# Kernel optimization log

Hardware: AMD Instinct MI355X
Metric: run time of the kernel (lower is better)

The kernel has to match this reference:

```python
import jax, jax.numpy as jnp
import numpy as np
from jax import lax

DS = 4  # downsample_factor

def setup_inputs() -> dict:
    key = jax.random.key(0)
    ks = jax.random.split(key, 7)
    B, C, H, W = 4, 256, 256, 256
    Cq = C // 16  # reduction=16
    return {
        "x":  jax.random.normal(ks[0], (B, C, H, W), dtype=jnp.float32),
        "Wq": jax.random.normal(ks[1], (Cq, C), dtype=jnp.float32) * 0.05,
        "bq": jax.random.normal(ks[2], (Cq,), dtype=jnp.float32) * 0.05,
        "Wk": jax.random.normal(ks[3], (Cq, C), dtype=jnp.float32) * 0.05,
        "bk": jax.random.normal(ks[4], (Cq,), dtype=jnp.float32) * 0.05,
        "Wv": jax.random.normal(ks[5], (C, C), dtype=jnp.float32) * 0.05,
        "bv": jax.random.normal(ks[6], (C,), dtype=jnp.float32) * 0.05,
    }

def reference(x, Wq, bq, Wk, bk, Wv, bv):
    B, C, H, W = x.shape
    # MaxPool2d(kernel=DS, stride=DS)
    xd = lax.reduce_window(x, -jnp.inf, lax.max,
                           (1, 1, DS, DS), (1, 1, DS, DS), 'VALID')
    h, w = xd.shape[2], xd.shape[3]
    N = h * w
    # 1x1 convs == channel-wise linear maps
    q = jnp.einsum('oc,bchw->bohw', Wq, xd) + bq[None, :, None, None]
    k = jnp.einsum('oc,bchw->bohw', Wk, xd) + bk[None, :, None, None]
    v = jnp.einsum('oc,bchw->bohw', Wv, xd) + bv[None, :, None, None]
    query = q.reshape(B, -1, N).transpose(0, 2, 1)   # [B, N, Cq]
    key_  = k.reshape(B, -1, N)                      # [B, Cq, N]
    value = v.reshape(B, C, N).transpose(0, 2, 1)    # [B, N, C]
    att = jnp.einsum('bnc,bcm->bnm', query, key_)    # [B, N, N]
    # global-mean threshold masking (zeros, not -inf, per original)
    att = jnp.where(att < att.mean(), 0.0, att)
    att = jax.nn.softmax(att, axis=-1)
    out = jnp.einsum('bnm,bmc->bnc', att, value)     # [B, N, C]
    out = out.transpose(0, 2, 1).reshape(B, C, h, w)
    # bilinear upsample, align_corners=False (half-pixel centers)
    out = jax.image.resize(out, (B, C, H, W), method='bilinear')
    return out + x
```

## Files before the change

kernel.cpp:

```cpp
#include <hip/hip_runtime.h>
#include <hip/hip_bf16.h>
#include <cmath>
#include <cstdint>
#include <cstddef>

typedef unsigned short u16;
typedef __attribute__((ext_vector_type(8))) __bf16 bf16x8;
typedef __attribute__((ext_vector_type(4))) float f32x4;
typedef __attribute__((ext_vector_type(8))) unsigned short us8;
typedef __attribute__((ext_vector_type(4))) unsigned short us4;

static const size_t OFF_XD32  = 0;
static const size_t OFF_QT    = 16777216;
static const size_t OFF_KT    = 17825792;
static const size_t OFF_VT    = 18874368;
static const size_t OFF_WF    = 27262976;
static const size_t OFF_SPART = 27394048;
static const size_t OFF_MEAN  = 27426816;

__device__ __forceinline__ void gl2lds16(const void* gsrc, void* ldst) {
  __builtin_amdgcn_global_load_lds(
      (const __attribute__((address_space(1))) unsigned int*)gsrc,
      (__attribute__((address_space(3))) unsigned int*)ldst, 16, 0, 0);
}

__device__ __forceinline__ float hmax4(float4 v) {
  return fmaxf(fmaxf(v.x, v.y), fmaxf(v.z, v.w));
}

__global__ __launch_bounds__(256) void k_prepw(const float* __restrict__ Wv,
                                               u16* __restrict__ Wf) {
  const int rt = blockIdx.x;
  const int tid = threadIdx.x;
#pragma unroll
  for (int i = 0; i < 2; ++i) {
    int s = tid + i * 256;
    int ks = s >> 6, lane = s & 63;
    const float* src = Wv + (size_t)(rt * 16 + (lane & 15)) * 256u + ks * 32 + (lane >> 4) * 8;
    float4 a = *reinterpret_cast<const float4*>(src);
    float4 b = *reinterpret_cast<const float4*>(src + 4);
    us8 o;
    o[0] = __builtin_bit_cast(u16, __float2bfloat16(a.x));
    o[1] = __builtin_bit_cast(u16, __float2bfloat16(a.y));
    o[2] = __builtin_bit_cast(u16, __float2bfloat16(a.z));
    o[3] = __builtin_bit_cast(u16, __float2bfloat16(a.w));
    o[4] = __builtin_bit_cast(u16, __float2bfloat16(b.x));
    o[5] = __builtin_bit_cast(u16, __float2bfloat16(b.y));
    o[6] = __builtin_bit_cast(u16, __float2bfloat16(b.z));
    o[7] = __builtin_bit_cast(u16, __float2bfloat16(b.w));
    *reinterpret_cast<us8*>(Wf + ((size_t)((rt * 8 + ks) * 64 + lane)) * 8u) = o;
  }
}

__global__ __launch_bounds__(256) void k_pool(const float* __restrict__ x,
                                              float* __restrict__ xd32) {
  unsigned idx = blockIdx.x * 256u + threadIdx.x;
  unsigned xo = idx & 63u;
  unsigned yo = (idx >> 6) & 63u;
  unsigned bc = idx >> 12;
  const float* base = x + (size_t)bc * 65536u + yo * 1024u + xo * 4u;
  float m = -1e30f;
#pragma unroll
  for (int dy = 0; dy < 4; ++dy) {
    float4 v = *reinterpret_cast<const float4*>(base + dy * 256);
    m = fmaxf(m, hmax4(v));
  }
  xd32[(size_t)bc * 4096u + yo * 64u + xo] = m;
}

__global__ __launch_bounds__(512) void k_qk(const float* __restrict__ xd32,
                                            const float* __restrict__ Wq, const float* __restrict__ bq,
                                            const float* __restrict__ Wk, const float* __restrict__ bk,
                                            float* __restrict__ qT, float* __restrict__ kT,
                                            float* __restrict__ Spart) {
  __shared__ float xs[256][64];
  const int blk = blockIdx.x;
  const int b = blk >> 6, n0 = (blk & 63) * 64;
  const int tid = threadIdx.x;
  {
    const float* src = xd32 + (size_t)b * 1048576u + n0;
#pragma unroll
    for (int i = 0; i < 8; ++i) {
      int slot = tid + i * 512;
      int c = slot >> 4, q4 = slot & 15;
      *reinterpret_cast<float4*>(&xs[c][q4 * 4]) =
          *reinterpret_cast<const float4*>(src + (size_t)c * 4096u + q4 * 4);
    }
  }
  __syncthreads();
  const int o = tid >> 4, t4 = tid & 15;
  const float* wrow = (o < 16) ? (Wq + (size_t)o * 256u) : (Wk + (size_t)(o - 16) * 256u);
  float a0 = 0.f, a1 = 0.f, a2 = 0.f, a3 = 0.f;
  for (int c = 0; c < 256; ++c) {
    float w = wrow[c];
    float4 xv = *reinterpret_cast<const float4*>(&xs[c][t4 * 4]);
    a0 = fmaf(w, xv.x, a0);
    a1 = fmaf(w, xv.y, a1);
    a2 = fmaf(w, xv.z, a2);
    a3 = fmaf(w, xv.w, a3);
  }
  float* dst = (o < 16) ? qT : kT;
  int oo = (o < 16) ? o : (o - 16);
  float bb = (o < 16) ? bq[oo] : bk[oo];
  size_t base = ((size_t)b * 4096u + n0 + t4 * 4) * 16u + oo;
  dst[base]      = a0 + bb;
  dst[base + 16] = a1 + bb;
  dst[base + 32] = a2 + bb;
  dst[base + 48] = a3 + bb;
  float s = a0 + a1 + a2 + a3;
  s += __shfl_xor(s, 1); s += __shfl_xor(s, 2);
  s += __shfl_xor(s, 4); s += __shfl_xor(s, 8);
  if (t4 == 0) Spart[(size_t)blk * 32u + o] = s;
}

__global__ __launch_bounds__(256) void k_vgemm(const float* __restrict__ xd32,
                                               const u16* __restrict__ Wf,
                                               const float* __restrict__ bv,
                                               u16* __restrict__ vT) {
  __shared__ u16 Bf[4][8][64][8];
  const int blk = blockIdx.x;
  const int b = blk >> 6, n0 = (blk & 63) * 64;
  const int tid = threadIdx.x;
  const int w = tid >> 6, lane = tid & 63;

#pragma unroll
  for (int p = 0; p < 16; ++p) {
    int idx = p * 256 + tid;
    int k = idx >> 4, q4 = idx & 15;
    float4 v = *reinterpret_cast<const float4*>(
        xd32 + ((size_t)b * 256 + k) * 4096u + n0 + q4 * 4);
    int ks = k >> 5, kl = (k >> 3) & 3, j = k & 7;
    int ct = q4 >> 2, nb = (q4 & 3) * 4;
    Bf[ct][ks][kl * 16 + nb + 0][j] = __builtin_bit_cast(u16, __float2bfloat16(v.x));
    Bf[ct][ks][kl * 16 + nb + 1][j] = __builtin_bit_cast(u16, __float2bfloat16(v.y));
    Bf[ct][ks][kl * 16 + nb + 2][j] = __builtin_bit_cast(u16, __float2bfloat16(v.z));
    Bf[ct][ks][kl * 16 + nb + 3][j] = __builtin_bit_cast(u16, __float2bfloat16(v.w));
  }
  __syncthreads();

  f32x4 acc[4][4];
#pragma unroll
  for (int r = 0; r < 4; ++r)
#pragma unroll
    for (int ct = 0; ct < 4; ++ct) acc[r][ct] = (f32x4){0.f, 0.f, 0.f, 0.f};
  for (int ks = 0; ks < 8; ++ks) {
    bf16x8 Bv[4];
#pragma unroll
    for (int ct = 0; ct < 4; ++ct)
      Bv[ct] = __builtin_bit_cast(bf16x8, *reinterpret_cast<const us8*>(&Bf[ct][ks][lane][0]));
#pragma unroll
    for (int r = 0; r < 4; ++r) {
      int rt = w * 4 + r;
      bf16x8 Av = __builtin_bit_cast(bf16x8,
          *reinterpret_cast<const us8*>(Wf + ((size_t)((rt * 8 + ks) * 64 + lane)) * 8u));
#pragma unroll
      for (int ct = 0; ct < 4; ++ct)
        acc[r][ct] = __builtin_amdgcn_mfma_f32_16x16x32_bf16(Av, Bv[ct], acc[r][ct], 0, 0, 0);
    }
  }

#pragma unroll
  for (int r = 0; r < 4; ++r) {
    int row0 = (w * 4 + r) * 16 + (lane >> 4) * 4;
#pragma unroll
    for (int rr = 0; rr < 4; ++rr) {
      int c = row0 + rr;
      float bb = bv[c];
      u16* dst = vT + ((size_t)b * 256 + c) * 4096u + n0 + (lane & 15);
#pragma unroll
      for (int ct = 0; ct < 4; ++ct)
        dst[ct * 16] = __builtin_bit_cast(u16, __float2bfloat16(acc[r][ct][rr] + bb));
    }
  }
}

__global__ __launch_bounds__(64) void k_mean(const float* __restrict__ Spart,
                                             const float* __restrict__ bq, const float* __restrict__ bk,
                                             float* __restrict__ meanp) {
  int t = threadIdx.x;
  int b = t >> 4, o = t & 15;
  float sq = 4096.0f * bq[o], sk = 4096.0f * bk[o];
  for (int blk = 0; blk < 64; ++blk) {
    const float* p = Spart + ((size_t)(b * 64 + blk)) * 32u;
    sq += p[o];
    sk += p[16 + o];
  }
  float pr = sq * sk;
#pragma unroll
  for (int off = 32; off > 0; off >>= 1) pr += __shfl_down(pr, off);
  if (t == 0) *meanp = pr * (1.0f / 67108864.0f);
}

__global__ __launch_bounds__(512) void k_flash(const float* __restrict__ qT,
                                               const float* __restrict__ kT,
                                               const u16* __restrict__ vT,
                                               const float* __restrict__ meanp,
                                               float* __restrict__ ods) {
  __shared__ u16 vbuf[2][16384];
  __shared__ u16 kfh[2][4][64][8];
  __shared__ u16 kfl[2][4][64][8];
  __shared__ u16 pfr[8][2][64][8];

  const int orig = blockIdx.x;
  const int b    = (orig >> 1) & 3;
  const int row0 = (((orig & 1) << 5) | (orig >> 3)) * 64;
  const int tid  = threadIdx.x;
  const int w    = tid >> 6;
  const int lane = tid & 63;
  const int wq   = w & 3;
  const int wc   = w >> 2;
  const int g    = lane >> 4;
  const int c16  = lane & 15;

  const float mean = *meanp;

  float qv[16];
  {
    const float* qrow = qT + ((size_t)b*4096 + row0 + 16*wq + c16) * 16;
#pragma unroll
    for (int i = 0; i < 4; ++i) {
      float4 t4 = reinterpret_cast<const float4*>(qrow)[i];
      qv[4*i] = t4.x; qv[4*i+1] = t4.y; qv[4*i+2] = t4.z; qv[4*i+3] = t4.w;
    }
  }
  u16 qhi[16], qlo[16];
#pragma unroll
  for (int i = 0; i < 16; ++i) {
    __hip_bfloat16 h = __float2bfloat16(qv[i]);
    float fh = __bfloat162float(h);
    __hip_bfloat16 lo = __float2bfloat16(qv[i] - fh);
    qhi[i] = __builtin_bit_cast(u16, h);
    qlo[i] = __builtin_bit_cast(u16, lo);
  }
  us8 a1u, a2u;
  {
    const bool koff8  = (g & 1);
    const bool lo_src = (g >= 2);
#pragma unroll
    for (int i = 0; i < 8; ++i) {
      u16 hs = koff8 ? qhi[i+8] : qhi[i];
      u16 ls = koff8 ? qlo[i+8] : qlo[i];
      a1u[i] = lo_src ? ls : hs;
      a2u[i] = lo_src ? (u16)0 : hs;
    }
  }
  const bf16x8 A1 = __builtin_bit_cast(bf16x8, a1u);
  const bf16x8 A2 = __builtin_bit_cast(bf16x8, a2u);

  f32x4 O[8];
#pragma unroll
  for (int i = 0; i < 8; ++i) O[i] = (f32x4){0.f, 0.f, 0.f, 0.f};
  float Lr[4] = {0.f, 0.f, 0.f, 0.f};
  float M = 0.0f;

  const int kv_s = tid >> 2, t4v = tid & 3;
  const int ks = kv_s >> 4, kld0 = (kv_s & 15) + 16*(t4v >> 1), ki0 = 4*(t4v & 1);

  {
    const u16* vsrc = vT + (size_t)b*256*4096;
#pragma unroll
    for (int i = 0; i < 4; ++i) {
      int u = i*512 + tid;
      int row = u >> 3, slot = u & 7;
      int sb = (slot*16) ^ ((row & 7) << 4);
      gl2lds16((const char*)(vsrc + (size_t)row*4096) + sb, (char*)&vbuf[0][0] + u*16);
    }
    if (tid < 256) {
      float4 kvec = *reinterpret_cast<const float4*>(kT + ((size_t)b*4096 + kv_s)*16 + 4*t4v);
      float kf[4] = {kvec.x, kvec.y, kvec.z, kvec.w};
      us4 h4, l4;
#pragma unroll
      for (int di = 0; di < 4; ++di) {
        __hip_bfloat16 h = __float2bfloat16(kf[di]);
        float fh = __bfloat162float(h);
        __hip_bfloat16 lo = __float2bfloat16(kf[di] - fh);
        h4[di] = __builtin_bit_cast(u16, h);
        l4[di] = __builtin_bit_cast(u16, lo);
      }
      *reinterpret_cast<us4*>(&kfh[0][ks][kld0][ki0])    = h4;
      *reinterpret_cast<us4*>(&kfh[0][ks][kld0+32][ki0]) = h4;
      *reinterpret_cast<us4*>(&kfl[0][ks][kld0][ki0])    = l4;
      *reinterpret_cast<us4*>(&kfl[0][ks][kld0+32][ki0]) = l4;
    }
  }
  __syncthreads();

  for (int t = 0; t < 64; ++t) {
    const int cur = t & 1, nxt = cur ^ 1;
    const int kv0n = ((t + 1) & 63) * 64;

    float4 kvec;
    if (tid < 256)
      kvec = *reinterpret_cast<const float4*>(kT + ((size_t)b*4096 + kv0n + kv_s)*16 + 4*t4v);
    {
      const u16* vsrc = vT + (size_t)b*256*4096 + kv0n;
#pragma unroll
      for (int i = 0; i < 4; ++i) {
        int u = i*512 + tid;
        int row = u >> 3, slot = u & 7;
        int sb = (slot*16) ^ ((row & 7) << 4);
        gl2lds16((const char*)(vsrc + (size_t)row*4096) + sb, (char*)&vbuf[nxt][0] + u*16);
      }
    }

    f32x4 S[4];
#pragma unroll
    for (int s = 0; s < 4; ++s) {
      bf16x8 bh = __builtin_bit_cast(bf16x8, *reinterpret_cast<const us8*>(&kfh[cur][s][lane][0]));
      bf16x8 bl = __builtin_bit_cast(bf16x8, *reinterpret_cast<const us8*>(&kfl[cur][s][lane][0]));
      f32x4 acc = (f32x4){0.f, 0.f, 0.f, 0.f};
      acc = __builtin_amdgcn_mfma_f32_16x16x32_bf16(A1, bh, acc, 0, 0, 0);
      acc = __builtin_amdgcn_mfma_f32_16x16x32_bf16(A2, bl, acc, 0, 0, 0);
      S[s] = acc;
    }

    float pmax = -1e30f;
#pragma unroll
    for (int s = 0; s < 4; ++s)
#pragma unroll
      for (int r = 0; r < 4; ++r) {
        float v = S[s][r];
        v = (v < mean) ? 0.f : v;
        S[s][r] = v;
        pmax = fmaxf(pmax, v);
      }
    if (!__all(pmax <= M + 8.0f)) {
      float mw = pmax;
#pragma unroll
      for (int off = 1; off < 64; off <<= 1) mw = fmaxf(mw, __shfl_xor(mw, off));
      float Mn = fmaxf(M, mw);
      float sc = __expf(M - Mn);
#pragma unroll
      for (int i = 0; i < 8; ++i) {
        O[i][0] *= sc; O[i][1] *= sc; O[i][2] *= sc; O[i][3] *= sc;
      }
#pragma unroll
      for (int r = 0; r < 4; ++r) Lr[r] *= sc;
      M = Mn;
    }
    u16 pb[4][4];
#pragma unroll
    for (int s = 0; s < 4; ++s)
#pragma unroll
      for (int r = 0; r < 4; ++r) {
        float p = __expf(S[s][r] - M);
        Lr[r] += p;
        pb[s][r] = __builtin_bit_cast(u16, __float2bfloat16(p));
      }

    {
      const int ib = lane & 7;
      const int t1 = (lane >> 3) & 1;
#pragma unroll
      for (int s = 0; s < 4; ++s) {
        const int c2 = s >> 1;
        const int ldb = 16 * ((2*s + t1) & 3) + 4*g;
#pragma unroll
        for (int r = 0; r < 4; ++r) pfr[w][c2][ldb + r][ib] = pb[s][r];
      }
    }
    asm volatile("s_waitcnt lgkmcnt(0)" ::: "memory");
    __builtin_amdgcn_sched_barrier(0);

#pragma unroll
    for (int c2 = 0; c2 < 2; ++c2) {
      bf16x8 pa = __builtin_bit_cast(bf16x8, *reinterpret_cast<const us8*>(&pfr[w][c2][lane][0]));
#pragma unroll
      for (int ct = 0; ct < 8; ++ct) {
        int row = (wc*8 + ct)*16 + c16;
        int off = (c2*64 + g*16) ^ ((lane & 7) << 4);
        bf16x8 vb = __builtin_bit_cast(bf16x8,
            *reinterpret_cast<const us8*>((const char*)&vbuf[cur][0] + row*128 + off));
        O[ct] = __builtin_amdgcn_mfma_f32_16x16x32_bf16(pa, vb, O[ct], 0, 0, 0);
      }
    }

    if (tid < 256) {
      float kf[4] = {kvec.x, kvec.y, kvec.z, kvec.w};
      us4 h4, l4;
#pragma unroll
      for (int di = 0; di < 4; ++di) {
        __hip_bfloat16 h = __float2bfloat16(kf[di]);
        float fh = __bfloat162float(h);
        __hip_bfloat16 lo = __float2bfloat16(kf[di] - fh);
        h4[di] = __builtin_bit_cast(u16, h);
        l4[di] = __builtin_bit_cast(u16, lo);
      }
      *reinterpret_cast<us4*>(&kfh[nxt][ks][kld0][ki0])    = h4;
      *reinterpret_cast<us4*>(&kfh[nxt][ks][kld0+32][ki0]) = h4;
      *reinterpret_cast<us4*>(&kfl[nxt][ks][kld0][ki0])    = l4;
      *reinterpret_cast<us4*>(&kfl[nxt][ks][kld0+32][ki0]) = l4;
    }

    __syncthreads();
  }

#pragma unroll
  for (int r = 0; r < 4; ++r) {
    float v = Lr[r];
#pragma unroll
    for (int off = 1; off < 16; off <<= 1) v += __shfl_xor(v, off);
    Lr[r] = v;
  }
  float inv[4];
#pragma unroll
  for (int r = 0; r < 4; ++r) inv[r] = 1.0f / Lr[r];
#pragma unroll
  for (int ct = 0; ct < 8; ++ct) {
    int c = (wc*8 + ct)*16 + c16;
    float* dst = ods + ((size_t)b*256 + c) * 4096u + row0 + 16*wq + 4*g;
    float4 o4 = make_float4(O[ct][0]*inv[0], O[ct][1]*inv[1], O[ct][2]*inv[2], O[ct][3]*inv[3]);
    *reinterpret_cast<float4*>(dst) = o4;
  }
}

__global__ __launch_bounds__(256) void k_up(const float* __restrict__ ods, const float* __restrict__ x,
                                            float* __restrict__ out) {
  unsigned idx4 = blockIdx.x * 256u + threadIdx.x;
  int a  = (int)(idx4 & 63u);
  int i  = (int)((idx4 >> 6) & 255u);
  size_t bc = idx4 >> 14;

  float py = (i + 0.5f) * 0.25f - 0.5f;
  float y0f = floorf(py);
  float wy = py - y0f;
  int y0 = (int)y0f, y1 = y0 + 1;
  y0 = max(y0, 0); y1 = min(y1, 63);

  int xm1 = max(a - 1, 0), xp1 = min(a + 1, 63);

  const float* r0 = ods + bc * 4096u + y0 * 64;
  const float* r1 = ods + bc * 4096u + y1 * 64;
  float wy1 = 1.f - wy;
  float vm1 = wy1 * r0[xm1] + wy * r1[xm1];
  float v0  = wy1 * r0[a]   + wy * r1[a];
  float vp1 = wy1 * r0[xp1] + wy * r1[xp1];

  float4 xv = *reinterpret_cast<const float4*>(x + (size_t)idx4 * 4u);
  float4 o4;
  o4.x = fmaf(0.375f, vm1, 0.625f * v0) + xv.x;
  o4.y = fmaf(0.125f, vm1, 0.875f * v0) + xv.y;
  o4.z = fmaf(0.875f, v0, 0.125f * vp1) + xv.z;
  o4.w = fmaf(0.625f, v0, 0.375f * vp1) + xv.w;
  *reinterpret_cast<float4*>(out + (size_t)idx4 * 4u) = o4;
}

extern "C" void kernel_launch(void* const* d_in, const int* in_sizes, int n_in,
                              void* d_out, int out_size, void* d_ws, size_t ws_size,
                              hipStream_t stream) {
  const float* x  = (const float*)d_in[0];
  const float* Wq = (const float*)d_in[1];
  const float* bq = (const float*)d_in[2];
  const float* Wk = (const float*)d_in[3];
  const float* bk = (const float*)d_in[4];
  const float* Wv = (const float*)d_in[5];
  const float* bv = (const float*)d_in[6];
  float* out = (float*)d_out;

  char* ws = (char*)d_ws;
  float* xd32  = (float*)(ws + OFF_XD32);
  float* qT    = (float*)(ws + OFF_QT);
  float* kT    = (float*)(ws + OFF_KT);
  u16*   vT    = (u16*)(ws + OFF_VT);
  u16*   Wf    = (u16*)(ws + OFF_WF);
  float* Spart = (float*)(ws + OFF_SPART);
  float* mnp   = (float*)(ws + OFF_MEAN);
  float* ods   = xd32;

  k_prepw<<<dim3(16), dim3(256), 0, stream>>>(Wv, Wf);
  k_pool<<<dim3(16384), dim3(256), 0, stream>>>(x, xd32);
  k_qk<<<dim3(256), dim3(512), 0, stream>>>(xd32, Wq, bq, Wk, bk, qT, kT, Spart);
  k_vgemm<<<dim3(256), dim3(256), 0, stream>>>(xd32, Wf, bv, vT);
  k_mean<<<dim3(1), dim3(64), 0, stream>>>(Spart, bq, bk, mnp);
  k_flash<<<dim3(256), dim3(512), 0, stream>>>(qT, kT, vT, mnp, ods);
  k_up<<<dim3(65536), dim3(256), 0, stream>>>(ods, x, out);
}
```

Before: 286.6 us.

## Merge QK and V projection kernels and fold mean reduction into flash kernel

Combines the Q/K projection and V GEMM into one launch of 512 blocks, with the first 256 blocks doing V (now 512 threads, two row tiles per wave) and the rest doing Q/K. The separate single-block mean kernel is removed, and each flash block recomputes the global mean from the partial sums in shared memory. This is meant to cut two kernel launches and the tiny serial mean kernel, and to let the two projections run concurrently. In exchange, every flash block redundantly reads the partial sums, and the merged kernel reserves 64KB of shared memory for the V blocks, which needed less before, which may lower occupancy.

```diff
diff --git a/kernel.cpp b/kernel.cpp
--- a/kernel.cpp
+++ b/kernel.cpp
@@ -16,7 +16,6 @@
 static const size_t OFF_VT    = 18874368;
 static const size_t OFF_WF    = 27262976;
 static const size_t OFF_SPART = 27394048;
-static const size_t OFF_MEAN  = 27426816;
 
 __device__ __forceinline__ void gl2lds16(const void* gsrc, void* ldst) {
   __builtin_amdgcn_global_load_lds(
@@ -68,138 +67,123 @@
   xd32[(size_t)bc * 4096u + yo * 64u + xo] = m;
 }
 
-__global__ __launch_bounds__(512) void k_qk(const float* __restrict__ xd32,
-                                            const float* __restrict__ Wq, const float* __restrict__ bq,
-                                            const float* __restrict__ Wk, const float* __restrict__ bk,
-                                            float* __restrict__ qT, float* __restrict__ kT,
-                                            float* __restrict__ Spart) {
-  __shared__ float xs[256][64];
-  const int blk = blockIdx.x;
-  const int b = blk >> 6, n0 = (blk & 63) * 64;
+__global__ __launch_bounds__(512) void k_qkv(const float* __restrict__ xd32,
+                                             const u16* __restrict__ Wf, const float* __restrict__ bv,
+                                             const float* __restrict__ Wq, const float* __restrict__ bq,
+                                             const float* __restrict__ Wk, const float* __restrict__ bk,
+                                             float* __restrict__ qT, float* __restrict__ kT,
+                                             u16* __restrict__ vT, float* __restrict__ Spart) {
+  __shared__ char smem[65536];
   const int tid = threadIdx.x;
-  {
-    const float* src = xd32 + (size_t)b * 1048576u + n0;
-#pragma unroll
-    for (int i = 0; i < 8; ++i) {
-      int slot = tid + i * 512;
-      int c = slot >> 4, q4 = slot & 15;
-      *reinterpret_cast<float4*>(&xs[c][q4 * 4]) =
-          *reinterpret_cast<const float4*>(src + (size_t)c * 4096u + q4 * 4);
-    }
-  }
-  __syncthreads();
-  const int o = tid >> 4, t4 = tid & 15;
-  const float* wrow = (o < 16) ? (Wq + (size_t)o * 256u) : (Wk + (size_t)(o - 16) * 256u);
-  float a0 = 0.f, a1 = 0.f, a2 = 0.f, a3 = 0.f;
-  for (int c = 0; c < 256; ++c) {
-    float w = wrow[c];
-    float4 xv = *reinterpret_cast<const float4*>(&xs[c][t4 * 4]);
-    a0 = fmaf(w, xv.x, a0);
-    a1 = fmaf(w, xv.y, a1);
-    a2 = fmaf(w, xv.z, a2);
-    a3 = fmaf(w, xv.w, a3);
-  }
-  float* dst = (o < 16) ? qT : kT;
-  int oo = (o < 16) ? o : (o - 16);
-  float bb = (o < 16) ? bq[oo] : bk[oo];
-  size_t base = ((size_t)b * 4096u + n0 + t4 * 4) * 16u + oo;
-  dst[base]      = a0 + bb;
-  dst[base + 16] = a1 + bb;
-  dst[base + 32] = a2 + bb;
-  dst[base + 48] = a3 + bb;
-  float s = a0 + a1 + a2 + a3;
-  s += __shfl_xor(s, 1); s += __shfl_xor(s, 2);
-  s += __shfl_xor(s, 4); s += __shfl_xor(s, 8);
-  if (t4 == 0) Spart[(size_t)blk * 32u + o] = s;
-}
-
-__global__ __launch_bounds__(256) void k_vgemm(const float* __restrict__ xd32,
-                                               const u16* __restrict__ Wf,
-                                               const float* __restrict__ bv,
-                                               u16* __restrict__ vT) {
-  __shared__ u16 Bf[4][8][64][8];
-  const int blk = blockIdx.x;
-  const int b = blk >> 6, n0 = (blk & 63) * 64;
-  const int tid = threadIdx.x;
-  const int w = tid >> 6, lane = tid & 63;
-
-#pragma unroll
-  for (int p = 0; p < 16; ++p) {
-    int idx = p * 256 + tid;
-    int k = idx >> 4, q4 = idx & 15;
-    float4 v = *reinterpret_cast<const float4*>(
-        xd32 + ((size_t)b * 256 + k) * 4096u + n0 + q4 * 4);
-    int ks = k >> 5, kl = (k >> 3) & 3, j = k & 7;
-    int ct = q4 >> 2, nb = (q4 & 3) * 4;
-    Bf[ct][ks][kl * 16 + nb + 0][j] = __builtin_bit_cast(u16, __float2bfloat16(v.x));
-    Bf[ct][ks][kl * 16 + nb + 1][j] = __builtin_bit_cast(u16, __float2bfloat16(v.y));
-    Bf[ct][ks][kl * 16 + nb + 2][j] = __builtin_bit_cast(u16, __float2bfloat16(v.z));
-    Bf[ct][ks][kl * 16 + nb + 3][j] = __builtin_bit_cast(u16, __float2bfloat16(v.w));
-  }
-  __syncthreads();
-
-  f32x4 acc[4][4];
-#pragma unroll
-  for (int r = 0; r < 4; ++r)
-#pragma unroll
-    for (int ct = 0; ct < 4; ++ct) acc[r][ct] = (f32x4){0.f, 0.f, 0.f, 0.f};
-  for (int ks = 0; ks < 8; ++ks) {
-    bf16x8 Bv[4];
-#pragma unroll
-    for (int ct = 0; ct < 4; ++ct)
-      Bv[ct] = __builtin_bit_cast(bf16x8, *reinterpret_cast<const us8*>(&Bf[ct][ks][lane][0]));
-#pragma unroll
-    for (int r = 0; r < 4; ++r) {
-      int rt = w * 4 + r;
-      bf16x8 Av = __builtin_bit_cast(bf16x8,
-          *reinterpret_cast<const us8*>(Wf + ((size_t)((rt * 8 + ks) * 64 + lane)) * 8u));
+
+  if (blockIdx.x < 256) {
+    u16 (*Bf)[8][64][8] = reinterpret_cast<u16(*)[8][64][8]>(smem);
+    const int blk = blockIdx.x;
+    const int b = blk >> 6, n0 = (blk & 63) * 64;
+    const int w = tid >> 6, lane = tid & 63;
+
+#pragma unroll
+    for (int p = 0; p < 8; ++p) {
+      int idx = p * 512 + tid;
+      int k = idx >> 4, q4 = idx & 15;
+      float4 v = *reinterpret_cast<const float4*>(
+          xd32 + ((size_t)b * 256 + k) * 4096u + n0 + q4 * 4);
+      int ks = k >> 5, kl = (k >> 3) & 3, j = k & 7;
+      int ct = q4 >> 2, nb = (q4 & 3) * 4;
+      Bf[ct][ks][kl * 16 + nb + 0][j] = __builtin_bit_cast(u16, __float2bfloat16(v.x));
+      Bf[ct][ks][kl * 16 + nb + 1][j] = __builtin_bit_cast(u16, __float2bfloat16(v.y));
+      Bf[ct][ks][kl * 16 + nb + 2][j] = __builtin_bit_cast(u16, __float2bfloat16(v.z));
+      Bf[ct][ks][kl * 16 + nb + 3][j] = __builtin_bit_cast(u16, __float2bfloat16(v.w));
+    }
+    __syncthreads();
+
+    f32x4 acc[2][4];
+#pragma unroll
+    for (int r = 0; r < 2; ++r)
+#pragma unroll
+      for (int ct = 0; ct < 4; ++ct) acc[r][ct] = (f32x4){0.f, 0.f, 0.f, 0.f};
+    for (int ks = 0; ks < 8; ++ks) {
+      bf16x8 Bv[4];
 #pragma unroll
       for (int ct = 0; ct < 4; ++ct)
-        acc[r][ct] = __builtin_amdgcn_mfma_f32_16x16x32_bf16(Av, Bv[ct], acc[r][ct], 0, 0, 0);
-    }
-  }
-
-#pragma unroll
-  for (int r = 0; r < 4; ++r) {
-    int row0 = (w * 4 + r) * 16 + (lane >> 4) * 4;
-#pragma unroll
-    for (int rr = 0; rr < 4; ++rr) {
-      int c = row0 + rr;
-      float bb = bv[c];
-      u16* dst = vT + ((size_t)b * 256 + c) * 4096u + n0 + (lane & 15);
-#pragma unroll
-      for (int ct = 0; ct < 4; ++ct)
-        dst[ct * 16] = __builtin_bit_cast(u16, __float2bfloat16(acc[r][ct][rr] + bb));
-    }
-  }
-}
-
-__global__ __launch_bounds__(64) void k_mean(const float* __restrict__ Spart,
-                                             const float* __restrict__ bq, const float* __restrict__ bk,
-                                             float* __restrict__ meanp) {
-  int t = threadIdx.x;
-  int b = t >> 4, o = t & 15;
-  float sq = 4096.0f * bq[o], sk = 4096.0f * bk[o];
-  for (int blk = 0; blk < 64; ++blk) {
-    const float* p = Spart + ((size_t)(b * 64 + blk)) * 32u;
-    sq += p[o];
-    sk += p[16 + o];
-  }
-  float pr = sq * sk;
-#pragma unroll
-  for (int off = 32; off > 0; off >>= 1) pr += __shfl_down(pr, off);
-  if (t == 0) *meanp = pr * (1.0f / 67108864.0f);
+        Bv[ct] = __builtin_bit_cast(bf16x8, *reinterpret_cast<const us8*>(&Bf[ct][ks][lane][0]));
+#pragma unroll
+      for (int r = 0; r < 2; ++r) {
+        int rt = w * 2 + r;
+        bf16x8 Av = __builtin_bit_cast(bf16x8,
+            *reinterpret_cast<const us8*>(Wf + ((size_t)((rt * 8 + ks) * 64 + lane)) * 8u));
+#pragma unroll
+        for (int ct = 0; ct < 4; ++ct)
+          acc[r][ct] = __builtin_amdgcn_mfma_f32_16x16x32_bf16(Av, Bv[ct], acc[r][ct], 0, 0, 0);
+      }
+    }
+
+#pragma unroll
+    for (int r = 0; r < 2; ++r) {
+      int row0 = (w * 2 + r) * 16 + (lane >> 4) * 4;
+#pragma unroll
+      for (int rr = 0; rr < 4; ++rr) {
+        int c = row0 + rr;
+        float bb = bv[c];
+        u16* dst = vT + ((size_t)b * 256 + c) * 4096u + n0 + (lane & 15);
+#pragma unroll
+        for (int ct = 0; ct < 4; ++ct)
+          dst[ct * 16] = __builtin_bit_cast(u16, __float2bfloat16(acc[r][ct][rr] + bb));
+      }
+    }
+  } else {
+    float (*xs)[64] = reinterpret_cast<float(*)[64]>(smem);
+    const int qb = blockIdx.x - 256;
+    const int b = qb >> 6, n0 = (qb & 63) * 64;
+    {
+      const float* src = xd32 + (size_t)b * 1048576u + n0;
+#pragma unroll
+      for (int i = 0; i < 8; ++i) {
+        int slot = tid + i * 512;
+        int c = slot >> 4, q4 = slot & 15;
+        *reinterpret_cast<float4*>(&xs[c][q4 * 4]) =
+            *reinterpret_cast<const float4*>(src + (size_t)c * 4096u + q4 * 4);
+      }
+    }
+    __syncthreads();
+    const int o = tid >> 4, t4 = tid & 15;
+    const float* wrow = (o < 16) ? (Wq + (size_t)o * 256u) : (Wk + (size_t)(o - 16) * 256u);
+    float a0 = 0.f, a1 = 0.f, a2 = 0.f, a3 = 0.f;
+    for (int c = 0; c < 256; ++c) {
+      float w = wrow[c];
+      float4 xv = *reinterpret_cast<const float4*>(&xs[c][t4 * 4]);
+      a0 = fmaf(w, xv.x, a0);
+      a1 = fmaf(w, xv.y, a1);
+      a2 = fmaf(w, xv.z, a2);
+      a3 = fmaf(w, xv.w, a3);
+    }
+    float* dst = (o < 16) ? qT : kT;
+    int oo = (o < 16) ? o : (o - 16);
+    float bb = (o < 16) ? bq[oo] : bk[oo];
+    size_t base = ((size_t)b * 4096u + n0 + t4 * 4) * 16u + oo;
+    dst[base]      = a0 + bb;
+    dst[base + 16] = a1 + bb;
+    dst[base + 32] = a2 + bb;
+    dst[base + 48] = a3 + bb;
+    float s = a0 + a1 + a2 + a3;
+    s += __shfl_xor(s, 1); s += __shfl_xor(s, 2);
+    s += __shfl_xor(s, 4); s += __shfl_xor(s, 8);
+    if (t4 == 0) Spart[(size_t)qb * 32u + o] = s;
+  }
 }
 
 __global__ __launch_bounds__(512) void k_flash(const float* __restrict__ qT,
                                                const float* __restrict__ kT,
                                                const u16* __restrict__ vT,
-                                               const float* __restrict__ meanp,
+                                               const float* __restrict__ Spart,
+                                               const float* __restrict__ bq,
+                                               const float* __restrict__ bk,
                                                float* __restrict__ ods) {
   __shared__ u16 vbuf[2][16384];
   __shared__ u16 kfh[2][4][64][8];
   __shared__ u16 kfl[2][4][64][8];
   __shared__ u16 pfr[8][2][64][8];
+  __shared__ float mean_s;
 
   const int orig = blockIdx.x;
   const int b    = (orig >> 1) & 3;
@@ -212,7 +196,19 @@
   const int g    = lane >> 4;
   const int c16  = lane & 15;
 
-  const float mean = *meanp;
+  if (tid < 64) {
+    int bb = tid >> 4, o = tid & 15;
+    float sq = 4096.0f * bq[o], sk = 4096.0f * bk[o];
+    for (int s = 0; s < 64; ++s) {
+      const float* p = Spart + ((size_t)(bb * 64 + s)) * 32u;
+      sq += p[o];
+      sk += p[16 + o];
+    }
+    float pr = sq * sk;
+#pragma unroll
+    for (int off = 32; off > 0; off >>= 1) pr += __shfl_down(pr, off);
+    if (tid == 0) mean_s = pr * (1.0f / 67108864.0f);
+  }
 
   float qv[16];
   {
@@ -284,6 +280,7 @@
     }
   }
   __syncthreads();
+  const float mean = mean_s;
 
   for (int t = 0; t < 64; ++t) {
     const int cur = t & 1, nxt = cur ^ 1;
@@ -464,14 +461,11 @@
   u16*   vT    = (u16*)(ws + OFF_VT);
   u16*   Wf    = (u16*)(ws + OFF_WF);
   float* Spart = (float*)(ws + OFF_SPART);
-  float* mnp   = (float*)(ws + OFF_MEAN);
   float* ods   = xd32;
 
   k_prepw<<<dim3(16), dim3(256), 0, stream>>>(Wv, Wf);
   k_pool<<<dim3(16384), dim3(256), 0, stream>>>(x, xd32);
-  k_qk<<<dim3(256), dim3(512), 0, stream>>>(xd32, Wq, bq, Wk, bk, qT, kT, Spart);
-  k_vgemm<<<dim3(256), dim3(256), 0, stream>>>(xd32, Wf, bv, vT);
-  k_mean<<<dim3(1), dim3(64), 0, stream>>>(Spart, bq, bk, mnp);
-  k_flash<<<dim3(256), dim3(512), 0, stream>>>(qT, kT, vT, mnp, ods);
+  k_qkv<<<dim3(512), dim3(512), 0, stream>>>(xd32, Wf, bv, Wq, bq, Wk, bk, qT, kT, vT, Spart);
+  k_flash<<<dim3(256), dim3(512), 0, stream>>>(qT, kT, vT, Spart, bq, bk, ods);
   k_up<<<dim3(65536), dim3(256), 0, stream>>>(ods, x, out);
 }
```

After: 280.8 us. 2.0% less time.
